# Performance work log

Hardware: AMD Instinct MI355X
Metric: run time of the kernel (lower is better)

The kernel has to match this reference:

```python
import jax, jax.numpy as jnp
import numpy as np

N, E = 50000, 800000
F_IN, HID, HEADS, OUT, NG = 128, 32, 4, 64, 64
HD = HID * HEADS  # 128


def gat_layer(x, src, dst, W, a_s, a_d, b, heads, out_c):
    n = x.shape[0]
    h = (x @ W).reshape(n, heads, out_c)                      # [N,H,C]
    al_s = jnp.einsum('nhc,hc->nh', h, a_s)                   # [N,H]
    al_d = jnp.einsum('nhc,hc->nh', h, a_d)
    e = jax.nn.leaky_relu(al_s[src] + al_d[dst], 0.2)         # [E,H]
    m = jax.ops.segment_max(e, dst, num_segments=n)
    ex = jnp.exp(e - m[dst])
    s = jax.ops.segment_sum(ex, dst, num_segments=n)
    alpha = ex / (s[dst] + 1e-16)                             # [E,H]
    msg = h[src] * alpha[:, :, None]                          # [E,H,C]
    out = jax.ops.segment_sum(msg, dst, num_segments=n)       # [N,H,C]
    return out.reshape(n, heads * out_c) + b


def batchnorm(x, g, be, eps=1e-5):
    mu = x.mean(0)
    var = x.var(0)
    return (x - mu) * jax.lax.rsqrt(var + eps) * g + be


def setup_inputs():
    key = jax.random.key(0)
    ks = jax.random.split(key, 32)
    inp = {}
    inp['x'] = jax.random.normal(ks[0], (N, F_IN), dtype=jnp.float32)
    inp['edge_index'] = jax.random.randint(ks[1], (2, E), 0, N, dtype=jnp.int64)
    inp['batch_ids'] = jnp.sort(jax.random.randint(ks[2], (N,), 0, NG, dtype=jnp.int64))
    dims = [(F_IN, HEADS, HID), (HD, HEADS, HID), (HD, HEADS, HID), (HD, 1, OUT)]
    for i, (din, h, c) in enumerate(dims):
        sc = 1.0 / np.sqrt(din)
        inp[f'W{i}'] = jax.random.normal(ks[3 + 4 * i], (din, h * c), dtype=jnp.float32) * sc
        inp[f'as{i}'] = jax.random.normal(ks[4 + 4 * i], (h, c), dtype=jnp.float32) * 0.1
        inp[f'ad{i}'] = jax.random.normal(ks[5 + 4 * i], (h, c), dtype=jnp.float32) * 0.1
        inp[f'b{i}'] = jnp.zeros((h * c,), dtype=jnp.float32)
    for i in range(3):
        inp[f'g{i}'] = jnp.ones((HD,), dtype=jnp.float32)
        inp[f'be{i}'] = jnp.zeros((HD,), dtype=jnp.float32)
    return inp


def reference(x, edge_index, batch_ids,
              W0, as0, ad0, b0, W1, as1, ad1, b1,
              W2, as2, ad2, b2, W3, as3, ad3, b3,
              g0, be0, g1, be1, g2, be2):
    # add self-loops (PyG GATConv default)
    loop = jnp.arange(N, dtype=edge_index.dtype)
    src = jnp.concatenate([edge_index[0], loop])
    dst = jnp.concatenate([edge_index[1], loop])

    h = x
    layers = [(W0, as0, ad0, b0, g0, be0), (W1, as1, ad1, b1, g1, be1),
              (W2, as2, ad2, b2, g2, be2)]
    for (W, a_s, a_d, b, g, be) in layers:
        h = gat_layer(h, src, dst, W, a_s, a_d, b, HEADS, HID)
        h = jax.nn.elu(batchnorm(h, g, be))
        # dropout p=0.6 is identity at inference
    h = gat_layer(h, src, dst, W3, as3, ad3, b3, 1, OUT)     # [N,OUT]

    # global mean pool over graphs
    ones = jnp.ones((N,), dtype=h.dtype)
    cnt = jax.ops.segment_sum(ones, batch_ids, num_segments=NG)
    summed = jax.ops.segment_sum(h, batch_ids, num_segments=NG)
    return summed / jnp.maximum(cnt, 1.0)[:, None]           # [NG,OUT]
```

## Files before the change

### kernel.cpp

```cpp
#include <hip/hip_runtime.h>

#define DEVINL __device__ __forceinline__

constexpr int N_NODES = 50000;
constexpr int E_EDGES = 800000;
constexpr int HD      = 128;
constexpr int NG      = 64;
constexpr int OUTC    = 64;
constexpr int NPAR    = 22;
constexpr int PAR_TOTAL = 3*(16384+3*128) + (8192+3*64) + 6*128;
constexpr int WT_TOTAL = 3*128*128 + 64*128;
constexpr int NB      = (N_NODES + 1023) / 1024;
constexpr int EBC     = 2048;
constexpr int NBLKC   = (E_EDGES + EBC - 1) / EBC;

typedef _Float16 half8_t __attribute__((ext_vector_type(8)));
typedef _Float16 half4_t __attribute__((ext_vector_type(4)));
typedef float    float4_t __attribute__((ext_vector_type(4)));

DEVINL float bf2f(unsigned short u){
  union { unsigned int i; float f; } v; v.i = ((unsigned int)u) << 16; return v.f;
}
DEVINL float lrelu(float v){ return v > 0.f ? v : 0.2f * v; }

__global__ void k_detect(const unsigned short* __restrict__ x,
                         const int* __restrict__ ei, int* __restrict__ flags){
  __shared__ int s_f32, s_i64;
  int t = threadIdx.x;
  if (t == 0){ s_f32 = 0; s_i64 = 1; }
  __syncthreads();
  for (int i = t; i < 2048; i += 256){
    float v = bf2f(x[i]);
    if (!(fabsf(v) < 1e4f)) s_f32 = 1;
  }
  for (int i = t; i < 512; i += 256){
    if (ei[2 * i + 1] != 0) s_i64 = 0;
  }
  __syncthreads();
  if (t == 0){ flags[0] = s_i64; flags[1] = s_f32; }
}

struct PtrTab { const void* p[NPAR]; int off[NPAR + 1]; };

__global__ void k_prep(PtrTab tab, const int* __restrict__ flags,
                       float* __restrict__ dst,
                       const void* __restrict__ W0, const void* __restrict__ W1,
                       const void* __restrict__ W2, const void* __restrict__ W3,
                       _Float16* __restrict__ wt16){
  int f = flags[1];
  int i = blockIdx.x * 256 + threadIdx.x;
  if (i < PAR_TOTAL){
    int k = 0;
    while (tab.off[k + 1] <= i) k++;
    int j = i - tab.off[k];
    dst[i] = f ? ((const float*)tab.p[k])[j] : bf2f(((const unsigned short*)tab.p[k])[j]);
    return;
  }
  int w = i - PAR_TOTAL;
  if (w >= WT_TOTAL) return;
  const void* W; int base, Mt;
  if (w < 49152){ int l = w >> 14; base = w & 16383; Mt = 128; W = (l == 0) ? W0 : (l == 1 ? W1 : W2); }
  else { base = w - 49152; Mt = 64; W = W3; }
  int nn = base >> 7, k = base & 127;
  float val = f ? ((const float*)W)[(size_t)k * Mt + nn]
                : bf2f(((const unsigned short*)W)[(size_t)k * Mt + nn]);
  wt16[w] = (_Float16)val;
}

__global__ __launch_bounds__(256) void k_count(const int* __restrict__ ei,
                      const int* __restrict__ flags, int* __restrict__ cntmat){
  __shared__ int cnt[NB];
  int t = threadIdx.x, blk = blockIdx.x;
  if (t < NB) cnt[t] = 0;
  __syncthreads();
  int f = flags[0];
  int e0 = blk * EBC;
  #pragma unroll
  for (int j = 0; j < EBC / 256; j++){
    int e = e0 + t + j * 256;
    if (e < E_EDGES){
      int d = ei[(size_t)(E_EDGES + e) << f];
      atomicAdd(&cnt[d >> 10], 1);
    }
  }
  __syncthreads();
  if (t < NB) cntmat[blk * NB + t] = cnt[t];
}

__global__ void k_scanmat(const int* __restrict__ cntmat, int* __restrict__ gbase,
                          int* __restrict__ bbase){
  __shared__ int cbase[NB + 1];
  __shared__ int csum[NB];
  int t = threadIdx.x;
  int s = 0;
  if (t < NB){
    for (int blk = 0; blk < NBLKC; blk++) s += cntmat[blk * NB + t];
    csum[t] = s;
  }
  __syncthreads();
  if (t == 0){
    int run = 0;
    for (int b = 0; b < NB; b++){ cbase[b] = run; run += csum[b]; }
    cbase[NB] = run;
  }
  __syncthreads();
  if (t <= NB) bbase[t] = cbase[t];
  if (t < NB){
    int run = cbase[t];
    for (int blk = 0; blk < NBLKC; blk++){
      gbase[blk * NB + t] = run;
      run += cntmat[blk * NB + t];
    }
  }
}

__global__ __launch_bounds__(256) void k_binscatter(const int* __restrict__ ei,
                      const int* __restrict__ flags, const int* __restrict__ gbase,
                      unsigned int* __restrict__ ebuf2){
  __shared__ int cur[NB];
  int t = threadIdx.x, blk = blockIdx.x;
  if (t < NB) cur[t] = gbase[blk * NB + t];
  __syncthreads();
  int f = flags[0];
  int e0 = blk * EBC;
  #pragma unroll
  for (int j = 0; j < EBC / 256; j++){
    int e = e0 + t + j * 256;
    if (e < E_EDGES){
      int s = ei[(size_t)e << f];
      int d = ei[(size_t)(E_EDGES + e) << f];
      int p = atomicAdd(&cur[d >> 10], 1);
      ebuf2[p] = (unsigned int)s | ((unsigned int)d << 16);
    }
  }
}

__global__ __launch_bounds__(256) void k_csrD(const unsigned int* __restrict__ ebuf2,
                      const int* __restrict__ bbase, int* __restrict__ offs,
                      int* __restrict__ ssrc, int n){
  __shared__ int hist[1024];
  __shared__ int wsum[256];
  int t = threadIdx.x, b = blockIdx.x;
  int nbase = b << 10;
  int s0 = bbase[b], s1 = bbase[b + 1];
  for (int i = t; i < 1024; i += 256) hist[i] = 0;
  __syncthreads();
  for (int i = s0 + t; i < s1; i += 256){
    unsigned int pk = ebuf2[i];
    atomicAdd(&hist[(int)(pk >> 16) - nbase], 1);
  }
  __syncthreads();
  int base4 = t * 4;
  int v0 = hist[base4], v1 = hist[base4 + 1], v2 = hist[base4 + 2], v3 = hist[base4 + 3];
  int s = v0 + v1 + v2 + v3;
  wsum[t] = s; __syncthreads();
  for (int off = 1; off < 256; off <<= 1){
    int x2 = (t >= off) ? wsum[t - off] : 0;
    __syncthreads();
    wsum[t] += x2;
    __syncthreads();
  }
  int run = s0 + wsum[t] - s;
  int node = nbase + base4;
  if (node < n) offs[node] = run;  hist[base4] = run;  run += v0;
  if (node + 1 < n) offs[node + 1] = run;  hist[base4 + 1] = run;  run += v1;
  if (node + 2 < n) offs[node + 2] = run;  hist[base4 + 2] = run;  run += v2;
  if (node + 3 < n) offs[node + 3] = run;  hist[base4 + 3] = run;
  if (b == NB - 1 && t == 255) offs[n] = s1;
  __syncthreads();
  for (int i = s0 + t; i < s1; i += 256){
    unsigned int pk = ebuf2[i];
    int p = atomicAdd(&hist[(int)(pk >> 16) - nbase], 1);
    ssrc[p] = (int)(pk & 0xFFFFu);
  }
}

template<int MT, bool FIRST>
__global__ __launch_bounds__(256) void k_gemm(
    const void* __restrict__ Ain, const int* __restrict__ flags,
    const float* __restrict__ bnsum, const float* __restrict__ bnsq,
    const float* __restrict__ g, const float* __restrict__ be,
    const _Float16* __restrict__ Wt16,
    const float* __restrict__ a_s, const float* __restrict__ a_d,
    _Float16* __restrict__ h16, float* __restrict__ als, float* __restrict__ ald,
    int n){
  __shared__ _Float16 AhL[64 * 136];
  __shared__ _Float16 WtL[MT * 72];
  __shared__ float scale[128], shift[128];
  const int t = threadIdx.x;
  const int rowBase = blockIdx.x * 64;
  if (!FIRST){
    if (t < 128){
      float inv_n = 1.f / (float)n;
      float mu = bnsum[t] * inv_n;
      float var = bnsq[t] * inv_n - mu * mu;
      float sc = g[t] * rsqrtf(var + 1e-5f);
      scale[t] = sc; shift[t] = be[t] - mu * sc;
    }
    __syncthreads();
  }
  for (int f = t; f < 64 * 16; f += 256){
    int r = f >> 4, c8 = (f & 15) << 3;
    int row = rowBase + r;
    float v[8];
    if (row < n){
      if (FIRST){
        if (flags[1]){
          float4 x0 = *(const float4*)((const float*)Ain + (size_t)row * 128 + c8);
          float4 x1 = *(const float4*)((const float*)Ain + (size_t)row * 128 + c8 + 4);
          v[0]=x0.x; v[1]=x0.y; v[2]=x0.z; v[3]=x0.w;
          v[4]=x1.x; v[5]=x1.y; v[6]=x1.z; v[7]=x1.w;
        } else {
          const unsigned short* xp = (const unsigned short*)Ain + (size_t)row * 128 + c8;
          ushort4 u0 = *(const ushort4*)xp; ushort4 u1 = *(const ushort4*)(xp + 4);
          v[0]=bf2f(u0.x); v[1]=bf2f(u0.y); v[2]=bf2f(u0.z); v[3]=bf2f(u0.w);
          v[4]=bf2f(u1.x); v[5]=bf2f(u1.y); v[6]=bf2f(u1.z); v[7]=bf2f(u1.w);
        }
      } else {
        half8_t a8 = *(const half8_t*)((const _Float16*)Ain + (size_t)row * 128 + c8);
        #pragma unroll
        for (int j = 0; j < 8; j++){
          float xv = (float)a8[j] * scale[c8 + j] + shift[c8 + j];
          v[j] = xv > 0.f ? xv : (__expf(xv) - 1.f);
        }
      }
    } else {
      #pragma unroll
      for (int j = 0; j < 8; j++) v[j] = 0.f;
    }
    half8_t h;
    #pragma unroll
    for (int j = 0; j < 8; j++) h[j] = (_Float16)v[j];
    *(half8_t*)&AhL[r * 136 + c8] = h;
  }
  const int lane = t & 63;
  const int m = lane & 15, quad = lane >> 4;
  const int band = (t >> 6) * 16;
  float4_t acc[MT / 16];
  #pragma unroll
  for (int ct = 0; ct < MT / 16; ct++) acc[ct] = (float4_t){0.f, 0.f, 0.f, 0.f};
  #pragma unroll
  for (int kh = 0; kh < 2; kh++){
    __syncthreads();
    for (int f = t; f < MT * 8; f += 256){
      int nn = f >> 3, c8 = (f & 7) << 3;
      *(half8_t*)&WtL[nn * 72 + c8] = *(const half8_t*)&Wt16[nn * 128 + kh * 64 + c8];
    }
    __syncthreads();
    half8_t a0 = *(half8_t*)&AhL[(band + m) * 136 + kh * 64 + quad * 8];
    half8_t a1 = *(half8_t*)&AhL[(band + m) * 136 + kh * 64 + 32 + quad * 8];
    #pragma unroll
    for (int ct = 0; ct < MT / 16; ct++){
      half8_t b0 = *(half8_t*)&WtL[(ct * 16 + m) * 72 + quad * 8];
      half8_t b1 = *(half8_t*)&WtL[(ct * 16 + m) * 72 + 32 + quad * 8];
      acc[ct] = __builtin_amdgcn_mfma_f32_16x16x32_f16(a0, b0, acc[ct], 0, 0, 0);
      acc[ct] = __builtin_amdgcn_mfma_f32_16x16x32_f16(a1, b1, acc[ct], 0, 0, 0);
    }
  }
  __syncthreads();
  #pragma unroll
  for (int ct = 0; ct < MT / 16; ct++)
    #pragma unroll
    for (int rg = 0; rg < 4; rg++)
      AhL[(band + quad * 4 + rg) * 136 + ct * 16 + m] = (_Float16)acc[ct][rg];
  __syncthreads();
  int r = t >> 2, q = t & 3;
  int row = rowBase + r;
  if (MT == 128){
    if (row < n){
      half8_t h0 = *(half8_t*)&AhL[r * 136 + q * 32];
      half8_t h1 = *(half8_t*)&AhL[r * 136 + q * 32 + 8];
      half8_t h2 = *(half8_t*)&AhL[r * 136 + q * 32 + 16];
      half8_t h3 = *(half8_t*)&AhL[r * 136 + q * 32 + 24];
      float pas = 0.f, pad = 0.f;
      #pragma unroll
      for (int j = 0; j < 8; j++){
        pas += (float)h0[j] * a_s[q * 32 + j]      + (float)h1[j] * a_s[q * 32 + 8 + j]
             + (float)h2[j] * a_s[q * 32 + 16 + j] + (float)h3[j] * a_s[q * 32 + 24 + j];
        pad += (float)h0[j] * a_d[q * 32 + j]      + (float)h1[j] * a_d[q * 32 + 8 + j]
             + (float)h2[j] * a_d[q * 32 + 16 + j] + (float)h3[j] * a_d[q * 32 + 24 + j];
      }
      als[(size_t)row * 4 + q] = pas;
      ald[(size_t)row * 4 + q] = pad;
      _Float16* hp = h16 + (size_t)row * 128 + q * 32;
      *(half8_t*)hp = h0; *(half8_t*)(hp + 8) = h1;
      *(half8_t*)(hp + 16) = h2; *(half8_t*)(hp + 24) = h3;
    }
  } else {
    half8_t h0 = *(half8_t*)&AhL[r * 136 + q * 16];
    half8_t h1 = *(half8_t*)&AhL[r * 136 + q * 16 + 8];
    float pas = 0.f, pad = 0.f;
    #pragma unroll
    for (int j = 0; j < 8; j++){
      pas += (float)h0[j] * a_s[q * 16 + j] + (float)h1[j] * a_s[q * 16 + 8 + j];
      pad += (float)h0[j] * a_d[q * 16 + j] + (float)h1[j] * a_d[q * 16 + 8 + j];
    }
    pas += __shfl_xor(pas, 1); pas += __shfl_xor(pas, 2);
    pad += __shfl_xor(pad, 1); pad += __shfl_xor(pad, 2);
    if (row < n){
      _Float16* hp = h16 + (size_t)row * 64 + q * 16;
      *(half8_t*)hp = h0; *(half8_t*)(hp + 8) = h1;
      if (q == 0){ als[row] = pas; ald[row] = pad; }
    }
  }
}

template<int H, int C, bool F16OUT>
__global__ __launch_bounds__(256) void k_attn(const _Float16* __restrict__ h16,
                      const float* __restrict__ als, const float* __restrict__ ald,
                      const int* __restrict__ offs, const int* __restrict__ ssrc,
                      const float* __restrict__ bias,
                      void* __restrict__ out, int n){
  constexpr int HC = H * C;
  constexpr int CPL = HC / 16;
  int node = blockIdx.x * 16 + (threadIdx.x >> 4);
  if (node >= n) return;
  int sub  = threadIdx.x & 15;
  int c0   = sub * CPL;
  int head = c0 / C;

  float ald_h = ald[(size_t)node * H + head];
  float acc[CPL];
  float ssum;
  {
    float w = __expf(lrelu(als[(size_t)node * H + head] + ald_h));
    ssum = w;
    const _Float16* hp = h16 + (size_t)node * HC + c0;
    #pragma unroll
    for (int i = 0; i < CPL; i++) acc[i] = w * (float)hp[i];
  }
  int beg = offs[node];
  int deg = offs[node + 1] - beg;
  int j = 0;
  for (; j + 4 <= deg; j += 4){
    int s0 = ssrc[beg + j], s1 = ssrc[beg + j + 1];
    int s2 = ssrc[beg + j + 2], s3 = ssrc[beg + j + 3];
    float al0 = als[(size_t)s0 * H + head], al1 = als[(size_t)s1 * H + head];
    float al2 = als[(size_t)s2 * H + head], al3 = als[(size_t)s3 * H + head];
    if constexpr (CPL == 8){
      half8_t v0 = *(const half8_t*)(h16 + (size_t)s0 * HC + c0);
      half8_t v1 = *(const half8_t*)(h16 + (size_t)s1 * HC + c0);
      half8_t v2 = *(const half8_t*)(h16 + (size_t)s2 * HC + c0);
      half8_t v3 = *(const half8_t*)(h16 + (size_t)s3 * HC + c0);
      float w0 = __expf(lrelu(al0 + ald_h)), w1 = __expf(lrelu(al1 + ald_h));
      float w2 = __expf(lrelu(al2 + ald_h)), w3 = __expf(lrelu(al3 + ald_h));
      ssum += (w0 + w1) + (w2 + w3);
      #pragma unroll
      for (int i = 0; i < 8; i++)
        acc[i] += w0 * (float)v0[i] + w1 * (float)v1[i]
                + w2 * (float)v2[i] + w3 * (float)v3[i];
    } else {
      half4_t v0 = *(const half4_t*)(h16 + (size_t)s0 * HC + c0);
      half4_t v1 = *(const half4_t*)(h16 + (size_t)s1 * HC + c0);
      half4_t v2 = *(const half4_t*)(h16 + (size_t)s2 * HC + c0);
      half4_t v3 = *(const half4_t*)(h16 + (size_t)s3 * HC + c0);
      float w0 = __expf(lrelu(al0 + ald_h)), w1 = __expf(lrelu(al1 + ald_h));
      float w2 = __expf(lrelu(al2 + ald_h)), w3 = __expf(lrelu(al3 + ald_h));
      ssum += (w0 + w1) + (w2 + w3);
      #pragma unroll
      for (int i = 0; i < 4; i++)
        acc[i] += w0 * (float)v0[i] + w1 * (float)v1[i]
                + w2 * (float)v2[i] + w3 * (float)v3[i];
    }
  }
  for (; j < deg; j++){
    int s0 = ssrc[beg + j];
    float al0 = als[(size_t)s0 * H + head];
    float w0 = __expf(lrelu(al0 + ald_h));
    ssum += w0;
    const _Float16* hp = h16 + (size_t)s0 * HC + c0;
    #pragma unroll
    for (int i = 0; i < CPL; i++) acc[i] += w0 * (float)hp[i];
  }
  float inv_s = 1.f / ssum;
  if constexpr (F16OUT){
    _Float16* op = (_Float16*)out + (size_t)node * HC + c0;
    half8_t o;
    #pragma unroll
    for (int i = 0; i < CPL; i++) o[i] = (_Float16)(acc[i] * inv_s + bias[c0 + i]);
    *(half8_t*)op = o;
  } else {
    float* op = (float*)out + (size_t)node * HC + c0;
    #pragma unroll
    for (int i = 0; i < CPL; i += 4){
      float4 o0 = make_float4(acc[i]*inv_s + bias[c0+i], acc[i+1]*inv_s + bias[c0+i+1],
                              acc[i+2]*inv_s + bias[c0+i+2], acc[i+3]*inv_s + bias[c0+i+3]);
      *(float4*)(op + i) = o0;
    }
  }
}

__global__ void k_bn_stats(const _Float16* __restrict__ A16, float* __restrict__ bsum,
                           float* __restrict__ bsq, int n){
  __shared__ float ls[256], lq[256];
  int t = threadIdx.x;
  int col = t & 127;
  int rhalf = t >> 7;
  float s = 0.f, q = 0.f;
  for (int r = blockIdx.x * 2 + rhalf; r < n; r += gridDim.x * 2){
    float v = (float)A16[(size_t)r * 128 + col];
    s += v; q += v * v;
  }
  ls[t] = s; lq[t] = q; __syncthreads();
  if (t < 128){
    s = ls[t] + ls[t + 128];
    q = lq[t] + lq[t + 128];
    atomicAdd(&bsum[col], s);
    atomicAdd(&bsq[col], q);
  }
}

__global__ void k_pool_acc(const float* __restrict__ A, const int* __restrict__ bids,
                           const int* __restrict__ flags, float* __restrict__ sums,
                           int* __restrict__ gcnt, int n){
  int t = threadIdx.x;
  int f = flags[0];
  int col = t & 63;
  int rsub = t >> 6;
  int r0 = blockIdx.x * 128;
  float acc = 0.f; int cnt = 0; int cur = -1;
  for (int i = 0; i < 32; i++){
    int r = r0 + rsub + i * 4;
    if (r >= n) break;
    int g = bids[(size_t)r << f];
    if (g != cur){
      if (cur >= 0){
        atomicAdd(&sums[cur * 64 + col], acc);
        if (col == 0) atomicAdd(&gcnt[cur], cnt);
      }
      cur = g; acc = 0.f; cnt = 0;
    }
    acc += A[(size_t)r * 64 + col];
    cnt++;
  }
  if (cur >= 0){
    atomicAdd(&sums[cur * 64 + col], acc);
    if (col == 0) atomicAdd(&gcnt[cur], cnt);
  }
}

__global__ void k_pool_fin(const float* __restrict__ sums, const int* __restrict__ gcnt,
                           float* __restrict__ out){
  int i = blockIdx.x * 256 + threadIdx.x;
  if (i >= NG * OUTC) return;
  int g = i >> 6;
  int cnt = gcnt[g];
  float c = (float)(cnt > 1 ? cnt : 1);
  out[i] = sums[i] / c;
}

extern "C" void kernel_launch(void* const* d_in, const int* in_sizes, int n_in,
                              void* d_out, int out_size, void* d_ws, size_t ws_size,
                              hipStream_t stream){
  const unsigned short* x    = (const unsigned short*)d_in[0];
  const int*            ei   = (const int*)d_in[1];
  const int*            bids = (const int*)d_in[2];

  char* p = (char*)d_ws;
  auto carve = [&](size_t bytes) -> void* {
    void* r = (void*)p; p += (bytes + 255) & ~size_t(255); return r;
  };
  _Float16* a16    = (_Float16*)carve((size_t)N_NODES * HD * 2);
  _Float16* h16    = (_Float16*)carve((size_t)N_NODES * HD * 2);
  float*    Afin   = (float*)carve((size_t)N_NODES * OUTC * 4);
  float*    par    = (float*)carve((size_t)PAR_TOTAL * 4);
  _Float16* wt16   = (_Float16*)carve((size_t)WT_TOTAL * 2);
  float*    als    = (float*)carve((size_t)N_NODES * 4 * 4);
  float*    ald    = (float*)carve((size_t)N_NODES * 4 * 4);
  int*      offs   = (int*)carve((size_t)(N_NODES + 1) * 4);
  int*      ssrc   = (int*)carve((size_t)E_EDGES * 4);
  unsigned int* ebuf2 = (unsigned int*)carve((size_t)E_EDGES * 4);
  int*      cntmat = (int*)carve((size_t)NBLKC * NB * 4);
  int*      gbase  = (int*)carve((size_t)NBLKC * NB * 4);
  int*      bbase  = (int*)carve((size_t)(NB + 1) * 4);
  int*      flags  = (int*)carve(256);
  char*     zbeg   = p;
  float*    bnbuf  = (float*)carve(3 * 1024);
  float*    psum   = (float*)carve(NG * OUTC * 4);
  int*      gcnt   = (int*)carve(256);
  size_t    zlen   = (size_t)(p - zbeg);

  PtrTab tab;
  int sizes[NPAR];
  for (int l = 0; l < 4; l++){
    int base = 3 + 4 * l;
    tab.p[4 * l + 0] = d_in[base + 0]; sizes[4 * l + 0] = (l < 3) ? 16384 : 8192;
    tab.p[4 * l + 1] = d_in[base + 1]; sizes[4 * l + 1] = (l < 3) ? 128 : 64;
    tab.p[4 * l + 2] = d_in[base + 2]; sizes[4 * l + 2] = (l < 3) ? 128 : 64;
    tab.p[4 * l + 3] = d_in[base + 3]; sizes[4 * l + 3] = (l < 3) ? 128 : 64;
  }
  for (int l = 0; l < 3; l++){
    tab.p[16 + 2 * l]     = d_in[19 + 2 * l];     sizes[16 + 2 * l] = 128;
    tab.p[16 + 2 * l + 1] = d_in[19 + 2 * l + 1]; sizes[16 + 2 * l + 1] = 128;
  }
  tab.off[0] = 0;
  for (int k = 0; k < NPAR; k++) tab.off[k + 1] = tab.off[k] + sizes[k];
  const float* pAS[4], *pAD[4], *pB[4], *pG[3], *pBE[3];
  for (int l = 0; l < 4; l++){
    pAS[l] = par + tab.off[4 * l + 1];
    pAD[l] = par + tab.off[4 * l + 2];
    pB[l]  = par + tab.off[4 * l + 3];
  }
  for (int l = 0; l < 3; l++){
    pG[l]  = par + tab.off[16 + 2 * l];
    pBE[l] = par + tab.off[16 + 2 * l + 1];
  }
  const _Float16* pWT[4] = { wt16, wt16 + 16384, wt16 + 32768, wt16 + 49152 };
  float* bnS[3], *bnQ[3];
  for (int l = 0; l < 3; l++){ bnS[l] = bnbuf + 256 * l; bnQ[l] = bnbuf + 256 * l + 128; }

  hipMemsetAsync(zbeg, 0, zlen, stream);

  k_detect<<<1, 256, 0, stream>>>(x, ei, flags);
  k_prep<<<(PAR_TOTAL + WT_TOTAL + 255) / 256, 256, 0, stream>>>(
      tab, flags, par, d_in[3], d_in[7], d_in[11], d_in[15], wt16);

  k_count<<<NBLKC, 256, 0, stream>>>(ei, flags, cntmat);
  k_scanmat<<<1, 256, 0, stream>>>(cntmat, gbase, bbase);
  k_binscatter<<<NBLKC, 256, 0, stream>>>(ei, flags, gbase, ebuf2);
  k_csrD<<<NB, 256, 0, stream>>>(ebuf2, bbase, offs, ssrc, N_NODES);

  int gemmBlocks = (N_NODES + 63) / 64;
  int attnBlocks = (N_NODES + 15) / 16;

  k_gemm<128, true><<<gemmBlocks, 256, 0, stream>>>(
      (const void*)x, flags, nullptr, nullptr, nullptr, nullptr,
      pWT[0], pAS[0], pAD[0], h16, als, ald, N_NODES);
  k_attn<4, 32, true><<<attnBlocks, 256, 0, stream>>>(h16, als, ald, offs, ssrc, pB[0],
                                                      (void*)a16, N_NODES);
  k_bn_stats<<<256, 256, 0, stream>>>(a16, bnS[0], bnQ[0], N_NODES);
  for (int l = 1; l < 3; l++){
    k_gemm<128, false><<<gemmBlocks, 256, 0, stream>>>(
        (const void*)a16, flags, bnS[l-1], bnQ[l-1], pG[l-1], pBE[l-1],
        pWT[l], pAS[l], pAD[l], h16, als, ald, N_NODES);
    k_attn<4, 32, true><<<attnBlocks, 256, 0, stream>>>(h16, als, ald, offs, ssrc, pB[l],
                                                        (void*)a16, N_NODES);
    k_bn_stats<<<256, 256, 0, stream>>>(a16, bnS[l], bnQ[l], N_NODES);
  }
  k_gemm<64, false><<<gemmBlocks, 256, 0, stream>>>(
      (const void*)a16, flags, bnS[2], bnQ[2], pG[2], pBE[2],
      pWT[3], pAS[3], pAD[3], h16, als, ald, N_NODES);
  k_attn<1, 64, false><<<attnBlocks, 256, 0, stream>>>(h16, als, ald, offs, ssrc, pB[3],
                                                       (void*)Afin, N_NODES);

  k_pool_acc<<<(N_NODES + 127) / 128, 256, 0, stream>>>(Afin, bids, flags, psum, gcnt, N_NODES);
  k_pool_fin<<<16, 256, 0, stream>>>(psum, gcnt, (float*)d_out);
}
```

Measured before the change: 511.6 us.

## Fuse BN statistics and mean-pool into attention kernels, merge detect into prep

```diff
diff --git a/kernel.cpp b/kernel.cpp
--- a/kernel.cpp
+++ b/kernel.cpp
@@ -13,6 +13,7 @@
 constexpr int NB      = (N_NODES + 1023) / 1024;
 constexpr int EBC     = 2048;
 constexpr int NBLKC   = (E_EDGES + EBC - 1) / EBC;
+constexpr int BNSLOTS = 16;
 
 typedef _Float16 half8_t __attribute__((ext_vector_type(8)));
 typedef _Float16 half4_t __attribute__((ext_vector_type(4)));
@@ -23,32 +24,30 @@
 }
 DEVINL float lrelu(float v){ return v > 0.f ? v : 0.2f * v; }
 
-__global__ void k_detect(const unsigned short* __restrict__ x,
-                         const int* __restrict__ ei, int* __restrict__ flags){
-  __shared__ int s_f32, s_i64;
-  int t = threadIdx.x;
-  if (t == 0){ s_f32 = 0; s_i64 = 1; }
-  __syncthreads();
-  for (int i = t; i < 2048; i += 256){
-    float v = bf2f(x[i]);
-    if (!(fabsf(v) < 1e4f)) s_f32 = 1;
-  }
-  for (int i = t; i < 512; i += 256){
-    if (ei[2 * i + 1] != 0) s_i64 = 0;
-  }
-  __syncthreads();
-  if (t == 0){ flags[0] = s_i64; flags[1] = s_f32; }
-}
-
 struct PtrTab { const void* p[NPAR]; int off[NPAR + 1]; };
 
-__global__ void k_prep(PtrTab tab, const int* __restrict__ flags,
+__global__ void k_prep(PtrTab tab, const unsigned short* __restrict__ x,
+                       const int* __restrict__ ei, int* __restrict__ flags,
                        float* __restrict__ dst,
                        const void* __restrict__ W0, const void* __restrict__ W1,
                        const void* __restrict__ W2, const void* __restrict__ W3,
                        _Float16* __restrict__ wt16){
-  int f = flags[1];
-  int i = blockIdx.x * 256 + threadIdx.x;
+  __shared__ int s_f32, s_i64;
+  int t = threadIdx.x;
+  if (t == 0){ s_f32 = 0; s_i64 = 1; }
+  __syncthreads();
+  for (int i = t; i < 2048; i += 256){
+    float v = bf2f(x[i]);
+    if (!(fabsf(v) < 1e4f)) s_f32 = 1;
+  }
+  for (int i = t; i < 512; i += 256){
+    if (ei[2 * i + 1] != 0) s_i64 = 0;
+  }
+  __syncthreads();
+  int f = s_f32;
+  if (blockIdx.x == 0 && t == 0){ flags[0] = s_i64; flags[1] = s_f32; }
+
+  int i = blockIdx.x * 256 + t;
   if (i < PAR_TOTAL){
     int k = 0;
     while (tab.off[k + 1] <= i) k++;
@@ -178,7 +177,7 @@
 template<int MT, bool FIRST>
 __global__ __launch_bounds__(256) void k_gemm(
     const void* __restrict__ Ain, const int* __restrict__ flags,
-    const float* __restrict__ bnsum, const float* __restrict__ bnsq,
+    const float* __restrict__ bnslots,
     const float* __restrict__ g, const float* __restrict__ be,
     const _Float16* __restrict__ Wt16,
     const float* __restrict__ a_s, const float* __restrict__ a_d,
@@ -191,9 +190,15 @@
   const int rowBase = blockIdx.x * 64;
   if (!FIRST){
     if (t < 128){
+      float s = 0.f, q = 0.f;
+      #pragma unroll
+      for (int sl = 0; sl < BNSLOTS; sl++){
+        s += bnslots[sl * 256 + t];
+        q += bnslots[sl * 256 + 128 + t];
+      }
       float inv_n = 1.f / (float)n;
-      float mu = bnsum[t] * inv_n;
-      float var = bnsq[t] * inv_n - mu * mu;
+      float mu = s * inv_n;
+      float var = q * inv_n - mu * mu;
       float sc = g[t] * rsqrtf(var + 1e-5f);
       scale[t] = sc; shift[t] = be[t] - mu * sc;
     }
@@ -305,17 +310,20 @@
   }
 }
 
-template<int H, int C, bool F16OUT>
+template<int H, int C, int MODE>
 __global__ __launch_bounds__(256) void k_attn(const _Float16* __restrict__ h16,
                       const float* __restrict__ als, const float* __restrict__ ald,
                       const int* __restrict__ offs, const int* __restrict__ ssrc,
                       const float* __restrict__ bias,
-                      void* __restrict__ out, int n){
+                      _Float16* __restrict__ a16out, float* __restrict__ bnout,
+                      const int* __restrict__ bids, const int* __restrict__ flags,
+                      float* __restrict__ psum, int* __restrict__ gcnt, int n){
   constexpr int HC = H * C;
   constexpr int CPL = HC / 16;
-  int node = blockIdx.x * 16 + (threadIdx.x >> 4);
-  if (node >= n) return;
-  int sub  = threadIdx.x & 15;
+  int t = threadIdx.x;
+  int nib  = t >> 4;
+  int node = blockIdx.x * 16 + nib;
+  int sub  = t & 15;
   int c0   = sub * CPL;
   int head = c0 / C;
 
@@ -332,19 +340,53 @@
   int beg = offs[node];
   int deg = offs[node + 1] - beg;
   int j = 0;
+  for (; j + 8 <= deg; j += 8){
+    int ss[8]; float al[8]; float w[8];
+    #pragma unroll
+    for (int u = 0; u < 8; u++) ss[u] = ssrc[beg + j + u];
+    #pragma unroll
+    for (int u = 0; u < 8; u++) al[u] = als[(size_t)ss[u] * H + head];
+    if constexpr (CPL == 8){
+      half8_t v[8];
+      #pragma unroll
+      for (int u = 0; u < 8; u++) v[u] = *(const half8_t*)(h16 + (size_t)ss[u] * HC + c0);
+      #pragma unroll
+      for (int u = 0; u < 8; u++){ w[u] = __expf(lrelu(al[u] + ald_h)); ssum += w[u]; }
+      #pragma unroll
+      for (int i = 0; i < 8; i++){
+        float a = 0.f;
+        #pragma unroll
+        for (int u = 0; u < 8; u++) a += w[u] * (float)v[u][i];
+        acc[i] += a;
+      }
+    } else {
+      half4_t v[8];
+      #pragma unroll
+      for (int u = 0; u < 8; u++) v[u] = *(const half4_t*)(h16 + (size_t)ss[u] * HC + c0);
+      #pragma unroll
+      for (int u = 0; u < 8; u++){ w[u] = __expf(lrelu(al[u] + ald_h)); ssum += w[u]; }
+      #pragma unroll
+      for (int i = 0; i < 4; i++){
+        float a = 0.f;
+        #pragma unroll
+        for (int u = 0; u < 8; u++) a += w[u] * (float)v[u][i];
+        acc[i] += a;
+      }
+    }
+  }
   for (; j + 4 <= deg; j += 4){
     int s0 = ssrc[beg + j], s1 = ssrc[beg + j + 1];
     int s2 = ssrc[beg + j + 2], s3 = ssrc[beg + j + 3];
     float al0 = als[(size_t)s0 * H + head], al1 = als[(size_t)s1 * H + head];
     float al2 = als[(size_t)s2 * H + head], al3 = als[(size_t)s3 * H + head];
+    float w0 = __expf(lrelu(al0 + ald_h)), w1 = __expf(lrelu(al1 + ald_h));
+    float w2 = __expf(lrelu(al2 + ald_h)), w3 = __expf(lrelu(al3 + ald_h));
+    ssum += (w0 + w1) + (w2 + w3);
     if constexpr (CPL == 8){
       half8_t v0 = *(const half8_t*)(h16 + (size_t)s0 * HC + c0);
       half8_t v1 = *(const half8_t*)(h16 + (size_t)s1 * HC + c0);
       half8_t v2 = *(const half8_t*)(h16 + (size_t)s2 * HC + c0);
       half8_t v3 = *(const half8_t*)(h16 + (size_t)s3 * HC + c0);
-      float w0 = __expf(lrelu(al0 + ald_h)), w1 = __expf(lrelu(al1 + ald_h));
-      float w2 = __expf(lrelu(al2 + ald_h)), w3 = __expf(lrelu(al3 + ald_h));
-      ssum += (w0 + w1) + (w2 + w3);
       #pragma unroll
       for (int i = 0; i < 8; i++)
         acc[i] += w0 * (float)v0[i] + w1 * (float)v1[i]
@@ -354,9 +396,6 @@
       half4_t v1 = *(const half4_t*)(h16 + (size_t)s1 * HC + c0);
       half4_t v2 = *(const half4_t*)(h16 + (size_t)s2 * HC + c0);
       half4_t v3 = *(const half4_t*)(h16 + (size_t)s3 * HC + c0);
-      float w0 = __expf(lrelu(al0 + ald_h)), w1 = __expf(lrelu(al1 + ald_h));
-      float w2 = __expf(lrelu(al2 + ald_h)), w3 = __expf(lrelu(al3 + ald_h));
-      ssum += (w0 + w1) + (w2 + w3);
       #pragma unroll
       for (int i = 0; i < 4; i++)
         acc[i] += w0 * (float)v0[i] + w1 * (float)v1[i]
@@ -365,88 +404,71 @@
   }
   for (; j < deg; j++){
     int s0 = ssrc[beg + j];
-    float al0 = als[(size_t)s0 * H + head];
-    float w0 = __expf(lrelu(al0 + ald_h));
+    float w0 = __expf(lrelu(als[(size_t)s0 * H + head] + ald_h));
     ssum += w0;
     const _Float16* hp = h16 + (size_t)s0 * HC + c0;
     #pragma unroll
     for (int i = 0; i < CPL; i++) acc[i] += w0 * (float)hp[i];
   }
   float inv_s = 1.f / ssum;
-  if constexpr (F16OUT){
-    _Float16* op = (_Float16*)out + (size_t)node * HC + c0;
+  float v[CPL];
+  #pragma unroll
+  for (int i = 0; i < CPL; i++) v[i] = acc[i] * inv_s + bias[c0 + i];
+
+  if constexpr (MODE == 0){
+    _Float16* op = a16out + (size_t)node * HC + c0;
     half8_t o;
     #pragma unroll
-    for (int i = 0; i < CPL; i++) o[i] = (_Float16)(acc[i] * inv_s + bias[c0 + i]);
+    for (int i = 0; i < CPL; i++) o[i] = (_Float16)v[i];
     *(half8_t*)op = o;
+    __shared__ float red[16][132];
+    *(float4*)&red[nib][c0]     = make_float4(v[0], v[1], v[2], v[3]);
+    *(float4*)&red[nib][c0 + 4] = make_float4(v[4], v[5], v[6], v[7]);
+    __syncthreads();
+    if (t < 128){
+      float s = 0.f, q = 0.f;
+      #pragma unroll
+      for (int i = 0; i < 16; i++){ float x = red[i][t]; s += x; q += x * x; }
+      int slot = blockIdx.x & (BNSLOTS - 1);
+      atomicAdd(&bnout[slot * 256 + t], s);
+      atomicAdd(&bnout[slot * 256 + 128 + t], q);
+    }
   } else {
-    float* op = (float*)out + (size_t)node * HC + c0;
-    #pragma unroll
-    for (int i = 0; i < CPL; i += 4){
-      float4 o0 = make_float4(acc[i]*inv_s + bias[c0+i], acc[i+1]*inv_s + bias[c0+i+1],
-                              acc[i+2]*inv_s + bias[c0+i+2], acc[i+3]*inv_s + bias[c0+i+3]);
-      *(float4*)(op + i) = o0;
-    }
-  }
-}
-
-__global__ void k_bn_stats(const _Float16* __restrict__ A16, float* __restrict__ bsum,
-                           float* __restrict__ bsq, int n){
-  __shared__ float ls[256], lq[256];
-  int t = threadIdx.x;
-  int col = t & 127;
-  int rhalf = t >> 7;
-  float s = 0.f, q = 0.f;
-  for (int r = blockIdx.x * 2 + rhalf; r < n; r += gridDim.x * 2){
-    float v = (float)A16[(size_t)r * 128 + col];
-    s += v; q += v * v;
-  }
-  ls[t] = s; lq[t] = q; __syncthreads();
-  if (t < 128){
-    s = ls[t] + ls[t + 128];
-    q = lq[t] + lq[t + 128];
-    atomicAdd(&bsum[col], s);
-    atomicAdd(&bsq[col], q);
-  }
-}
-
-__global__ void k_pool_acc(const float* __restrict__ A, const int* __restrict__ bids,
-                           const int* __restrict__ flags, float* __restrict__ sums,
-                           int* __restrict__ gcnt, int n){
-  int t = threadIdx.x;
-  int f = flags[0];
-  int col = t & 63;
-  int rsub = t >> 6;
-  int r0 = blockIdx.x * 128;
-  float acc = 0.f; int cnt = 0; int cur = -1;
-  for (int i = 0; i < 32; i++){
-    int r = r0 + rsub + i * 4;
-    if (r >= n) break;
-    int g = bids[(size_t)r << f];
-    if (g != cur){
-      if (cur >= 0){
-        atomicAdd(&sums[cur * 64 + col], acc);
-        if (col == 0) atomicAdd(&gcnt[cur], cnt);
+    __shared__ float pacc[2][64];
+    __shared__ int pcnt[2];
+    int f = flags[0];
+    if (t < 128) pacc[t >> 6][t & 63] = 0.f;
+    if (t < 2) pcnt[t] = 0;
+    __syncthreads();
+    int g  = (int)bids[(size_t)node << f];
+    int g0 = (int)bids[(size_t)(blockIdx.x * 16) << f];
+    int g1 = (int)bids[(size_t)(blockIdx.x * 16 + 15) << f];
+    if (g1 - g0 <= 1){
+      int gl = g - g0;
+      #pragma unroll
+      for (int i = 0; i < 4; i++) atomicAdd(&pacc[gl][c0 + i], v[i]);
+      if (sub == 0) atomicAdd(&pcnt[gl], 1);
+      __syncthreads();
+      if (t < 128){
+        int gl2 = t >> 6;
+        if (pcnt[gl2] > 0) atomicAdd(&psum[(g0 + gl2) * 64 + (t & 63)], pacc[gl2][t & 63]);
       }
-      cur = g; acc = 0.f; cnt = 0;
-    }
-    acc += A[(size_t)r * 64 + col];
-    cnt++;
-  }
-  if (cur >= 0){
-    atomicAdd(&sums[cur * 64 + col], acc);
-    if (col == 0) atomicAdd(&gcnt[cur], cnt);
-  }
-}
-
-__global__ void k_pool_fin(const float* __restrict__ sums, const int* __restrict__ gcnt,
+      if (t < 2 && pcnt[t] > 0) atomicAdd(&gcnt[g0 + t], pcnt[t]);
+    } else {
+      #pragma unroll
+      for (int i = 0; i < 4; i++) atomicAdd(&psum[g * 64 + c0 + i], v[i]);
+      if (sub == 0) atomicAdd(&gcnt[g], 1);
+      __syncthreads();
+    }
+  }
+}
+
+__global__ void k_pool_fin(const float* __restrict__ psum, const int* __restrict__ gcnt,
                            float* __restrict__ out){
   int i = blockIdx.x * 256 + threadIdx.x;
   if (i >= NG * OUTC) return;
-  int g = i >> 6;
-  int cnt = gcnt[g];
-  float c = (float)(cnt > 1 ? cnt : 1);
-  out[i] = sums[i] / c;
+  int cnt = gcnt[i >> 6];
+  out[i] = psum[i] / (float)(cnt > 1 ? cnt : 1);
 }
 
 extern "C" void kernel_launch(void* const* d_in, const int* in_sizes, int n_in,
@@ -462,7 +484,6 @@
   };
   _Float16* a16    = (_Float16*)carve((size_t)N_NODES * HD * 2);
   _Float16* h16    = (_Float16*)carve((size_t)N_NODES * HD * 2);
-  float*    Afin   = (float*)carve((size_t)N_NODES * OUTC * 4);
   float*    par    = (float*)carve((size_t)PAR_TOTAL * 4);
   _Float16* wt16   = (_Float16*)carve((size_t)WT_TOTAL * 2);
   float*    als    = (float*)carve((size_t)N_NODES * 4 * 4);
@@ -475,7 +496,7 @@
   int*      bbase  = (int*)carve((size_t)(NB + 1) * 4);
   int*      flags  = (int*)carve(256);
   char*     zbeg   = p;
-  float*    bnbuf  = (float*)carve(3 * 1024);
+  float*    bnbuf  = (float*)carve((size_t)3 * BNSLOTS * 256 * 4);
   float*    psum   = (float*)carve(NG * OUTC * 4);
   int*      gcnt   = (int*)carve(256);
   size_t    zlen   = (size_t)(p - zbeg);
@@ -506,14 +527,13 @@
     pBE[l] = par + tab.off[16 + 2 * l + 1];
   }
   const _Float16* pWT[4] = { wt16, wt16 + 16384, wt16 + 32768, wt16 + 49152 };
-  float* bnS[3], *bnQ[3];
-  for (int l = 0; l < 3; l++){ bnS[l] = bnbuf + 256 * l; bnQ[l] = bnbuf + 256 * l + 128; }
+  float* bnS[3];
+  for (int l = 0; l < 3; l++) bnS[l] = bnbuf + (size_t)l * BNSLOTS * 256;
 
   hipMemsetAsync(zbeg, 0, zlen, stream);
 
-  k_detect<<<1, 256, 0, stream>>>(x, ei, flags);
   k_prep<<<(PAR_TOTAL + WT_TOTAL + 255) / 256, 256, 0, stream>>>(
-      tab, flags, par, d_in[3], d_in[7], d_in[11], d_in[15], wt16);
+      tab, x, ei, flags, par, d_in[3], d_in[7], d_in[11], d_in[15], wt16);
 
   k_count<<<NBLKC, 256, 0, stream>>>(ei, flags, cntmat);
   k_scanmat<<<1, 256, 0, stream>>>(cntmat, gbase, bbase);
@@ -521,28 +541,25 @@
   k_csrD<<<NB, 256, 0, stream>>>(ebuf2, bbase, offs, ssrc, N_NODES);
 
   int gemmBlocks = (N_NODES + 63) / 64;
-  int attnBlocks = (N_NODES + 15) / 16;
+  int attnBlocks = N_NODES / 16;
 
   k_gemm<128, true><<<gemmBlocks, 256, 0, stream>>>(
-      (const void*)x, flags, nullptr, nullptr, nullptr, nullptr,
+      (const void*)x, flags, nullptr, nullptr, nullptr,
       pWT[0], pAS[0], pAD[0], h16, als, ald, N_NODES);
-  k_attn<4, 32, true><<<attnBlocks, 256, 0, stream>>>(h16, als, ald, offs, ssrc, pB[0],
-                                                      (void*)a16, N_NODES);
-  k_bn_stats<<<256, 256, 0, stream>>>(a16, bnS[0], bnQ[0], N_NODES);
+  k_attn<4, 32, 0><<<attnBlocks, 256, 0, stream>>>(h16, als, ald, offs, ssrc, pB[0],
+      a16, bnS[0], nullptr, nullptr, nullptr, nullptr, N_NODES);
   for (int l = 1; l < 3; l++){
     k_gemm<128, false><<<gemmBlocks, 256, 0, stream>>>(
-        (const void*)a16, flags, bnS[l-1], bnQ[l-1], pG[l-1], pBE[l-1],
+        (const void*)a16, flags, bnS[l-1], pG[l-1], pBE[l-1],
         pWT[l], pAS[l], pAD[l], h16, als, ald, N_NODES);
-    k_attn<4, 32, true><<<attnBlocks, 256, 0, stream>>>(h16, als, ald, offs, ssrc, pB[l],
-                                                        (void*)a16, N_NODES);
-    k_bn_stats<<<256, 256, 0, stream>>>(a16, bnS[l], bnQ[l], N_NODES);
+    k_attn<4, 32, 0><<<attnBlocks, 256, 0, stream>>>(h16, als, ald, offs, ssrc, pB[l],
+        a16, bnS[l], nullptr, nullptr, nullptr, nullptr, N_NODES);
   }
   k_gemm<64, false><<<gemmBlocks, 256, 0, stream>>>(
-      (const void*)a16, flags, bnS[2], bnQ[2], pG[2], pBE[2],
+      (const void*)a16, flags, bnS[2], pG[2], pBE[2],
       pWT[3], pAS[3], pAD[3], h16, als, ald, N_NODES);
-  k_attn<1, 64, false><<<attnBlocks, 256, 0, stream>>>(h16, als, ald, offs, ssrc, pB[3],
-                                                       (void*)Afin, N_NODES);
-
-  k_pool_acc<<<(N_NODES + 127) / 128, 256, 0, stream>>>(Afin, bids, flags, psum, gcnt, N_NODES);
+  k_attn<1, 64, 1><<<attnBlocks, 256, 0, stream>>>(h16, als, ald, offs, ssrc, pB[3],
+      nullptr, nullptr, bids, flags, psum, gcnt, N_NODES);
+
   k_pool_fin<<<16, 256, 0, stream>>>(psum, gcnt, (float*)d_out);
 }
```

Result: faster. 437.1 us (-14.6%).
